# Performance work log

Measured on AMD Instinct MI355X. Metric: run time of the kernel, lower is better.

## Reference

```python
import jax, jax.numpy as jnp
import numpy as np

N_GRIDS, N_FEATS = 64, 2
GD = GH = GW = 64
PE_TERMS, N_DIMS = 6, 3
NODES, N_OUT = 64, 1
N_PTS = 524288


def setup_inputs() -> dict:
    key = jax.random.key(0)
    ks = jax.random.split(key, 8)
    x = jax.random.uniform(ks[0], (N_PTS, N_DIMS), jnp.float32, -1.0, 1.0)
    grid_scales = jax.random.uniform(ks[1], (N_GRIDS, 3), jnp.float32, 1.0, 4.0)
    grid_translations = jax.random.uniform(ks[2], (N_GRIDS, 3), jnp.float32, -1.0, 1.0) * (grid_scales - 1.0)
    feature_grids = jax.random.normal(ks[3], (N_GRIDS, N_FEATS, GD, GH, GW), jnp.float32)
    d_in = PE_TERMS * N_DIMS * 2 + N_FEATS * N_GRIDS  # 36 + 128 = 164
    W0 = jax.random.normal(ks[4], (d_in, NODES), jnp.float32) * np.sqrt(2.0 / (d_in + NODES))
    b0 = jnp.zeros((NODES,), jnp.float32)
    W1 = jax.random.normal(ks[5], (NODES, NODES), jnp.float32) * np.sqrt(2.0 / (2 * NODES))
    b1 = jnp.zeros((NODES,), jnp.float32)
    W2 = jax.random.normal(ks[6], (NODES, N_OUT), jnp.float32) * np.sqrt(2.0 / (NODES + N_OUT))
    b2 = jnp.zeros((N_OUT,), jnp.float32)
    return dict(x=x, grid_scales=grid_scales, grid_translations=grid_translations,
                feature_grids=feature_grids, W0=W0, b0=b0, W1=W1, b1=b1, W2=W2, b2=b2)


def grid_sample_3d(vol, coords):
    """Trilinear grid_sample, align_corners=True, padding_mode='zeros'.
    vol: [C,D,H,W]; coords: [N,3] in (x,y,z) order (x -> W axis), range [-1,1].
    Returns [C,N]."""
    C, D, H, W = vol.shape
    flat = vol.reshape(C, D * H * W)
    ix = (coords[:, 0] + 1.0) * 0.5 * (W - 1)
    iy = (coords[:, 1] + 1.0) * 0.5 * (H - 1)
    iz = (coords[:, 2] + 1.0) * 0.5 * (D - 1)
    x0 = jnp.floor(ix); y0 = jnp.floor(iy); z0 = jnp.floor(iz)
    wx = ix - x0; wy = iy - y0; wz = iz - z0
    x0i = x0.astype(jnp.int32); y0i = y0.astype(jnp.int32); z0i = z0.astype(jnp.int32)
    out = jnp.zeros((C, coords.shape[0]), vol.dtype)
    for dz, wz_ in ((0, 1.0 - wz), (1, wz)):
        for dy, wy_ in ((0, 1.0 - wy), (1, wy)):
            for dx, wx_ in ((0, 1.0 - wx), (1, wx)):
                xi = x0i + dx; yi = y0i + dy; zi = z0i + dz
                valid = (xi >= 0) & (xi < W) & (yi >= 0) & (yi < H) & (zi >= 0) & (zi < D)
                idx = (jnp.clip(zi, 0, D - 1) * H + jnp.clip(yi, 0, H - 1)) * W + jnp.clip(xi, 0, W - 1)
                v = jnp.take(flat, idx, axis=1) * valid.astype(vol.dtype)[None, :]
                out = out + v * (wz_ * wy_ * wx_)[None, :]
    return out


def positional_encoding(x):
    # NeRF-style PE: sin/cos of pi*2^i * x, i in [0, PE_TERMS), out dim = 2*L*3
    freqs = jnp.pi * (2.0 ** jnp.arange(PE_TERMS, dtype=jnp.float32))  # [L]
    ang = x[:, None, :] * freqs[None, :, None]                          # [N,L,3]
    n = x.shape[0]
    return jnp.concatenate([jnp.sin(ang).reshape(n, -1), jnp.cos(ang).reshape(n, -1)], axis=1)


def snake_alt(x):
    return 0.5 * x + jnp.sin(x) ** 2


def reference(x, grid_scales, grid_translations, feature_grids, W0, b0, W1, b1, W2, b2):
    # per-grid affine transform (equivalent to bmm with the scale+translation 4x4)
    tp = x[None, :, :] * grid_scales[:, None, :] + grid_translations[:, None, :]  # [G,N,3]
    feats = jax.vmap(grid_sample_3d)(feature_grids, tp)  # [G,C,N]
    G, C, N = feats.shape
    feats = feats.reshape(G * C, N).T                    # [N, G*C]
    pe = positional_encoding(x)                          # [N, 2*L*3]
    y = jnp.concatenate([pe, feats], axis=1)
    y = snake_alt(y @ W0 + b0)
    y = snake_alt(y @ W1 + b1)
    y = y @ W2 + b2
    return y
```

## Files before the change

kernel.cpp:

```cpp
#include <hip/hip_runtime.h>
#include <hip/hip_bf16.h>

#define NPTS    524288
#define NG      64
#define GSZ     64
#define VOX     (GSZ*GSZ*GSZ)
#define NODES   64
#define TILE    64
#define NBLK    (NPTS / TILE)
#define K0      192
#define SF      200
#define WLCAP   2048
#define NCELL   4096

typedef __attribute__((ext_vector_type(8))) short bf16x8;
typedef __attribute__((ext_vector_type(4))) float f32x4;

__device__ inline unsigned short f2bf(float f) {
    __hip_bfloat16 b = __float2bfloat16(f);
    union { __hip_bfloat16 h; unsigned short u; } cv; cv.h = b;
    return cv.u;
}
__device__ inline unsigned int pk2(float c0, float c1) {
    return (unsigned int)f2bf(c0) | ((unsigned int)f2bf(c1) << 16);
}
__device__ inline float bflo(unsigned int v) { return __uint_as_float(v << 16); }
__device__ inline float bfhi(unsigned int v) { return __uint_as_float(v & 0xffff0000u); }

__device__ inline int spread4(int v) {
    return (v & 1) | ((v & 2) << 2) | ((v & 4) << 4) | ((v & 8) << 6);
}
__device__ inline int cell_of(float px, float py, float pz) {
    int cx = min(max((int)((px + 1.0f) * 8.0f), 0), 15);
    int cy = min(max((int)((py + 1.0f) * 8.0f), 0), 15);
    int cz = min(max((int)((pz + 1.0f) * 8.0f), 0), 15);
    return spread4(cx) | (spread4(cy) << 1) | (spread4(cz) << 2);
}

__global__ void vox_prep(const float* __restrict__ fg, uint4* __restrict__ vox4) {
    int idx = blockIdx.x * blockDim.x + threadIdx.x;
    int g = idx >> 16;
    int v = (idx & 65535) * 4;
    const float* base = fg + (size_t)g * (2 * VOX) + v;
    float4 a = *(const float4*)base;
    float4 b = *(const float4*)(base + VOX);
    vox4[idx] = make_uint4(pk2(a.x, b.x), pk2(a.y, b.y), pk2(a.z, b.z), pk2(a.w, b.w));
}

__global__ void w_prep(const float* __restrict__ W0, const float* __restrict__ W1,
                       unsigned short* __restrict__ w0t, unsigned short* __restrict__ w1t,
                       int* __restrict__ hist) {
    int t = blockIdx.x * blockDim.x + threadIdx.x;
    hist[t] = 0;
    for (int i = t; i < NODES * K0; i += 4096) {
        int n = i / K0, k = i - n * K0;
        w0t[i] = (k < 164) ? f2bf(W0[k * NODES + n]) : (unsigned short)0;
    }
    for (int i = t; i < NODES * NODES; i += 4096) {
        int n = i >> 6, k = i & 63;
        w1t[i] = f2bf(W1[k * NODES + n]);
    }
}

__global__ void sort_count(const float* __restrict__ x, unsigned short* __restrict__ cell_id,
                           int* __restrict__ hist) {
    int p = blockIdx.x * blockDim.x + threadIdx.x;
    int c = cell_of(x[p * 3 + 0], x[p * 3 + 1], x[p * 3 + 2]);
    cell_id[p] = (unsigned short)c;
    atomicAdd(&hist[c], 1);
}

__global__ void sort_scan(const int* __restrict__ hist, int* __restrict__ offs) {
    __shared__ int partial[256];
    int t = threadIdx.x;
    int loc[16];
    int s = 0;
    #pragma unroll
    for (int i = 0; i < 16; ++i) { loc[i] = s; s += hist[t * 16 + i]; }
    partial[t] = s;
    __syncthreads();
    for (int d = 1; d < 256; d <<= 1) {
        int v = (t >= d) ? partial[t - d] : 0;
        __syncthreads();
        partial[t] += v;
        __syncthreads();
    }
    int base = partial[t] - s;
    #pragma unroll
    for (int i = 0; i < 16; ++i) offs[t * 16 + i] = base + loc[i];
}

__global__ void sort_scatter(const float* __restrict__ x, const unsigned short* __restrict__ cell_id,
                             int* __restrict__ offs, float4* __restrict__ spts) {
    int p = blockIdx.x * blockDim.x + threadIdx.x;
    int c = cell_id[p];
    int pos = atomicAdd(&offs[c], 1);
    spts[pos] = make_float4(x[p * 3 + 0], x[p * 3 + 1], x[p * 3 + 2], __int_as_float(p));
}

__device__ inline void gather_pair(int pt, int g,
                                   const unsigned int* __restrict__ vox,
                                   const float* xs, const float* gss, const float* gts,
                                   unsigned short* Fsh) {
    float px = xs[pt * 3 + 0], py = xs[pt * 3 + 1], pz = xs[pt * 3 + 2];
    float ix = (px * gss[g * 3 + 0] + gts[g * 3 + 0] + 1.0f) * 31.5f;
    float iy = (py * gss[g * 3 + 1] + gts[g * 3 + 1] + 1.0f) * 31.5f;
    float iz = (pz * gss[g * 3 + 2] + gts[g * 3 + 2] + 1.0f) * 31.5f;
    float fx = floorf(ix), fy = floorf(iy), fz = floorf(iz);
    int x0 = (int)fx, y0 = (int)fy, z0 = (int)fz;
    float wx = ix - fx, wy = iy - fy, wz = iz - fz;
    float wxa0 = (x0 >= 0) ? (1.0f - wx) : 0.0f;
    float wxa1 = (x0 < 63) ? wx : 0.0f;
    float wya0 = (y0 >= 0) ? (1.0f - wy) : 0.0f;
    float wya1 = (y0 < 63) ? wy : 0.0f;
    float wza0 = (z0 >= 0) ? (1.0f - wz) : 0.0f;
    float wza1 = (z0 < 63) ? wz : 0.0f;
    int xc0 = max(x0, 0), xc1 = min(x0 + 1, 63);
    int yc0 = max(y0, 0), yc1 = min(y0 + 1, 63);
    int zc0 = max(z0, 0), zc1 = min(z0 + 1, 63);
    const unsigned int* vg = vox + ((size_t)g << 18);
    float f0 = 0.f, f1 = 0.f;
    #pragma unroll
    for (int dz = 0; dz < 2; ++dz) {
        int zc = dz ? zc1 : zc0; float wzv = dz ? wza1 : wza0;
        #pragma unroll
        for (int dy = 0; dy < 2; ++dy) {
            int yc = dy ? yc1 : yc0; float wyv = dy ? wya1 : wya0;
            int rowb = ((zc << 6) + yc) << 6;
            float wzy = wzv * wyv;
            unsigned int v0 = vg[rowb + xc0], v1 = vg[rowb + xc1];
            f0 += wzy * (wxa0 * bflo(v0) + wxa1 * bflo(v1));
            f1 += wzy * (wxa0 * bfhi(v0) + wxa1 * bfhi(v1));
        }
    }
    *(unsigned int*)&Fsh[pt * SF + 36 + 2 * g] = pk2(f0, f1);
}

__global__ void __launch_bounds__(256, 5)
amrsrn_main(const float4* __restrict__ spts,
            const float* __restrict__ gscale,
            const float* __restrict__ gtrans,
            const unsigned int* __restrict__ vox,
            const unsigned short* __restrict__ w0t,
            const unsigned short* __restrict__ w1t,
            const float* __restrict__ b0,
            const float* __restrict__ b1,
            const float* __restrict__ W2,
            const float* __restrict__ b2,
            float* __restrict__ out) {
    __shared__ unsigned short Fsh[TILE * SF];
    __shared__ unsigned short wl[WLCAP];
    __shared__ float xs[TILE * 3];
    __shared__ int   sidx[TILE];
    __shared__ float gss[NG * 3];
    __shared__ float gts[NG * 3];
    __shared__ int wl_cnt;

    const int tid = threadIdx.x;
    const int lane = tid & 63;
    const int cb = ((blockIdx.x & 7) << 10) | (blockIdx.x >> 3);
    const int base = cb * TILE;

    for (int i = tid; i < TILE * SF / 8; i += 256) ((uint4*)Fsh)[i] = make_uint4(0,0,0,0);
    if (tid < TILE) {
        float4 sp = spts[base + tid];
        xs[tid * 3 + 0] = sp.x; xs[tid * 3 + 1] = sp.y; xs[tid * 3 + 2] = sp.z;
        sidx[tid] = __float_as_int(sp.w);
    }
    if (tid < NG * 3) { gss[tid] = gscale[tid]; gts[tid] = gtrans[tid]; }
    if (tid == 0) wl_cnt = 0;
    __syncthreads();

    {
        int pt = tid & 63;
        int grp = tid >> 6;
        #pragma unroll
        for (int t = 0; t < 9; ++t) {
            int tau = grp * 9 + t;
            int tt = (tau < 18) ? tau : tau - 18;
            int l = tt / 3, d = tt - l * 3;
            float ang = xs[pt * 3 + d] * (3.14159265358979323846f * (float)(1 << l));
            float val = (tau < 18) ? __sinf(ang) : __cosf(ang);
            Fsh[pt * SF + tau] = f2bf(val);
        }
    }

    {
        int pt = tid & 63;
        int gbase = (tid >> 6) * 16;
        float px = xs[pt * 3 + 0], py = xs[pt * 3 + 1], pz = xs[pt * 3 + 2];
        for (int gi = 0; gi < 16; ++gi) {
            int g = gbase + gi;
            float ix = (px * gss[g * 3 + 0] + gts[g * 3 + 0] + 1.0f) * 31.5f;
            float iy = (py * gss[g * 3 + 1] + gts[g * 3 + 1] + 1.0f) * 31.5f;
            float iz = (pz * gss[g * 3 + 2] + gts[g * 3 + 2] + 1.0f) * 31.5f;
            bool valid = (ix >= -1.0f) & (ix < 64.0f)
                       & (iy >= -1.0f) & (iy < 64.0f)
                       & (iz >= -1.0f) & (iz < 64.0f);
            unsigned long long m = __ballot(valid);
            if (m) {
                int b = 0;
                if (lane == 0) b = atomicAdd(&wl_cnt, __popcll(m));
                b = __shfl(b, 0);
                if (valid) {
                    int slot = b + __popcll(m & ((1ull << lane) - 1ull));
                    if (slot < WLCAP) wl[slot] = (unsigned short)((pt << 6) | g);
                    else gather_pair(pt, g, vox, xs, gss, gts, Fsh);
                }
            }
        }
    }
    __syncthreads();

    {
        int n = min(wl_cnt, WLCAP);
        for (int i = tid; i < n; i += 256) {
            int e = wl[i];
            gather_pair(e >> 6, e & 63, vox, xs, gss, gts, Fsh);
        }
    }
    __syncthreads();

    const int wv = tid >> 6;
    const int ptb = wv * 16;
    const int row = lane & 15;
    const int quad = lane >> 4;
    const int koff = quad * 8;

    f32x4 acc0[4] = {{0,0,0,0},{0,0,0,0},{0,0,0,0},{0,0,0,0}};
    #pragma unroll
    for (int ks = 0; ks < 6; ++ks) {
        bf16x8 a = *(const bf16x8*)&Fsh[(ptb + row) * SF + ks * 32 + koff];
        #pragma unroll
        for (int nt = 0; nt < 4; ++nt) {
            bf16x8 b = *(const bf16x8*)&w0t[(nt * 16 + row) * K0 + ks * 32 + koff];
            acc0[nt] = __builtin_amdgcn_mfma_f32_16x16x32_bf16(a, b, acc0[nt], 0, 0, 0);
        }
    }
    #pragma unroll
    for (int nt = 0; nt < 4; ++nt) {
        int node = nt * 16 + row;
        float bb = b0[node];
        #pragma unroll
        for (int r = 0; r < 4; ++r) {
            float h = acc0[nt][r] + bb;
            float s = __sinf(h);
            h = 0.5f * h + s * s;
            Fsh[(ptb + quad * 4 + r) * SF + node] = f2bf(h);
        }
    }

    f32x4 acc1[4] = {{0,0,0,0},{0,0,0,0},{0,0,0,0},{0,0,0,0}};
    #pragma unroll
    for (int ks = 0; ks < 2; ++ks) {
        bf16x8 a = *(const bf16x8*)&Fsh[(ptb + row) * SF + ks * 32 + koff];
        #pragma unroll
        for (int nt = 0; nt < 4; ++nt) {
            bf16x8 b = *(const bf16x8*)&w1t[(nt * 16 + row) * NODES + ks * 32 + koff];
            acc1[nt] = __builtin_amdgcn_mfma_f32_16x16x32_bf16(a, b, acc1[nt], 0, 0, 0);
        }
    }
    float part[4] = {0.f, 0.f, 0.f, 0.f};
    #pragma unroll
    for (int nt = 0; nt < 4; ++nt) {
        int node = nt * 16 + row;
        float b1v = b1[node];
        float w2v = W2[node];
        #pragma unroll
        for (int r = 0; r < 4; ++r) {
            float h = acc1[nt][r] + b1v;
            float s = __sinf(h);
            h = 0.5f * h + s * s;
            part[r] += h * w2v;
        }
    }
    #pragma unroll
    for (int m = 1; m < 16; m <<= 1) {
        #pragma unroll
        for (int r = 0; r < 4; ++r) part[r] += __shfl_xor(part[r], m);
    }
    if (row == 0) {
        float b2v = b2[0];
        #pragma unroll
        for (int r = 0; r < 4; ++r) {
            int pt = ptb + quad * 4 + r;
            out[sidx[pt]] = part[r] + b2v;
        }
    }
}

__global__ void amrsrn_fallback(const float* __restrict__ x,
                                const float* __restrict__ gscale,
                                const float* __restrict__ gtrans,
                                const float* __restrict__ fg,
                                const float* __restrict__ W0,
                                const float* __restrict__ b0,
                                const float* __restrict__ W1,
                                const float* __restrict__ b1,
                                const float* __restrict__ W2,
                                const float* __restrict__ b2,
                                float* __restrict__ out) {
    int p = blockIdx.x * blockDim.x + threadIdx.x;
    float px = x[p*3+0], py = x[p*3+1], pz = x[p*3+2];
    float h0[NODES];
    #pragma unroll
    for (int j = 0; j < NODES; ++j) h0[j] = b0[j];
    #pragma unroll
    for (int l = 0; l < 6; ++l) {
        float freq = 3.14159265358979323846f * (float)(1 << l);
        #pragma unroll
        for (int d = 0; d < 3; ++d) {
            float v = (d == 0 ? px : (d == 1 ? py : pz)) * freq;
            float s = __sinf(v), c = __cosf(v);
            const float* wrs = W0 + (l*3 + d) * NODES;
            const float* wrc = W0 + (18 + l*3 + d) * NODES;
            #pragma unroll
            for (int j = 0; j < NODES; ++j) h0[j] += s * wrs[j] + c * wrc[j];
        }
    }
    for (int g = 0; g < NG; ++g) {
        float ix = (px * gscale[g*3+0] + gtrans[g*3+0] + 1.0f) * 31.5f;
        float iy = (py * gscale[g*3+1] + gtrans[g*3+1] + 1.0f) * 31.5f;
        float iz = (pz * gscale[g*3+2] + gtrans[g*3+2] + 1.0f) * 31.5f;
        float fxf = floorf(ix), fyf = floorf(iy), fzf = floorf(iz);
        int x0 = (int)fxf, y0 = (int)fyf, z0 = (int)fzf;
        float wx = ix - fxf, wy = iy - fyf, wz = iz - fzf;
        bool any = (x0 >= -1 && x0 < GSZ) && (y0 >= -1 && y0 < GSZ) && (z0 >= -1 && z0 < GSZ);
        if (any) {
            float f0 = 0.f, f1 = 0.f;
            #pragma unroll
            for (int dz = 0; dz < 2; ++dz) {
                int zi = z0 + dz; bool vz = ((unsigned)zi < (unsigned)GSZ);
                int zc = min(max(zi, 0), GSZ - 1);
                float wzf = dz ? wz : 1.f - wz;
                #pragma unroll
                for (int dy = 0; dy < 2; ++dy) {
                    int yi = y0 + dy; bool vy = ((unsigned)yi < (unsigned)GSZ);
                    int yc = min(max(yi, 0), GSZ - 1);
                    float wyf = dy ? wy : 1.f - wy;
                    int rowoff = (zc * GSZ + yc) * GSZ;
                    #pragma unroll
                    for (int dx = 0; dx < 2; ++dx) {
                        int xi = x0 + dx; bool vx = ((unsigned)xi < (unsigned)GSZ);
                        int xc = min(max(xi, 0), GSZ - 1);
                        float w = wzf * wyf * (dx ? wx : 1.f - wx);
                        w = (vz && vy && vx) ? w : 0.f;
                        const float* gp = fg + ((size_t)g << 19);
                        f0 += w * gp[rowoff + xc];
                        f1 += w * gp[VOX + rowoff + xc];
                    }
                }
            }
            const float* wr = W0 + (36 + 2*g) * NODES;
            #pragma unroll
            for (int j = 0; j < NODES; ++j) h0[j] += f0 * wr[j] + f1 * wr[NODES + j];
        }
    }
    #pragma unroll
    for (int j = 0; j < NODES; ++j) { float s = __sinf(h0[j]); h0[j] = 0.5f * h0[j] + s * s; }
    float out_acc = b2[0];
    #pragma unroll
    for (int half = 0; half < 2; ++half) {
        float h1[32];
        #pragma unroll
        for (int j = 0; j < 32; ++j) h1[j] = b1[half*32 + j];
        #pragma unroll
        for (int i = 0; i < NODES; ++i) {
            float a = h0[i];
            const float* w1r = W1 + i * NODES + half*32;
            #pragma unroll
            for (int j = 0; j < 32; ++j) h1[j] += a * w1r[j];
        }
        #pragma unroll
        for (int j = 0; j < 32; ++j) { float s = __sinf(h1[j]); out_acc += (0.5f * h1[j] + s * s) * W2[half*32 + j]; }
    }
    out[p] = out_acc;
}

extern "C" void kernel_launch(void* const* d_in, const int* in_sizes, int n_in,
                              void* d_out, int out_size, void* d_ws, size_t ws_size,
                              hipStream_t stream) {
    const float* x      = (const float*)d_in[0];
    const float* gscale = (const float*)d_in[1];
    const float* gtrans = (const float*)d_in[2];
    const float* fg     = (const float*)d_in[3];
    const float* W0     = (const float*)d_in[4];
    const float* b0     = (const float*)d_in[5];
    const float* W1     = (const float*)d_in[6];
    const float* b1     = (const float*)d_in[7];
    const float* W2     = (const float*)d_in[8];
    const float* b2     = (const float*)d_in[9];
    float* out = (float*)d_out;

    char* wsp = (char*)d_ws;
    unsigned short* w0t = (unsigned short*)wsp;
    unsigned short* w1t = w0t + NODES * K0;
    int* hist           = (int*)(wsp + (64 << 10));
    int* offs           = (int*)(wsp + (80 << 10));
    unsigned short* cid = (unsigned short*)(wsp + (96 << 10));
    float4* spts        = (float4*)(wsp + (96 << 10) + (1 << 20));
    unsigned int* vox   = (unsigned int*)(wsp + (96 << 10) + (1 << 20) + (8 << 20));
    const size_t ws_needed = (96 << 10) + (1 << 20) + (8 << 20) + (size_t)NG * VOX * 4;

    if (ws_size >= ws_needed) {
        vox_prep<<<(NG * VOX / 4) / 256, 256, 0, stream>>>(fg, (uint4*)vox);
        w_prep<<<16, 256, 0, stream>>>(W0, W1, w0t, w1t, hist);
        sort_count<<<NPTS / 256, 256, 0, stream>>>(x, cid, hist);
        sort_scan<<<1, 256, 0, stream>>>(hist, offs);
        sort_scatter<<<NPTS / 256, 256, 0, stream>>>(x, cid, offs, spts);
        amrsrn_main<<<NBLK, 256, 0, stream>>>(spts, gscale, gtrans, vox,
                                              w0t, w1t, b0, b1, W2, b2, out);
    } else {
        amrsrn_fallback<<<NPTS / 256, 256, 0, stream>>>(
            x, gscale, gtrans, fg, W0, b0, W1, b1, W2, b2, out);
    }
}
```

Baseline: 473.5 us.

## Replace per-point gather worklist with per-cell grid masks and batched gathers

Precomputes, for each of 4096 spatial cells, a 64-bit mask of which grids can overlap that cell. The main kernel ORs the masks over the tile's cell range and gathers only from those grids, dropping the per-point ballot/atomic worklist. Gathers are split into address prep, eight loads and math, and two pairs are issued together to raise memory-level parallelism. Launches are fused (weight prep with mask build, voxel packing with scatter) and the cell id is packed into the point index so the cid array is no longer needed. The tile-level union mask may include many grids that are invalid for individual points, so some useless gathers can be added.

```diff
diff --git a/kernel.cpp b/kernel.cpp
--- a/kernel.cpp
+++ b/kernel.cpp
@@ -10,7 +10,6 @@
 #define NBLK    (NPTS / TILE)
 #define K0      192
 #define SF      200
-#define WLCAP   2048
 #define NCELL   4096
 
 typedef __attribute__((ext_vector_type(8))) short bf16x8;
@@ -29,6 +28,9 @@
 
 __device__ inline int spread4(int v) {
     return (v & 1) | ((v & 2) << 2) | ((v & 4) << 4) | ((v & 8) << 6);
+}
+__device__ inline int compact4(int v) {
+    return (v & 1) | ((v >> 2) & 2) | ((v >> 4) & 4) | ((v >> 6) & 8);
 }
 __device__ inline int cell_of(float px, float py, float pz) {
     int cx = min(max((int)((px + 1.0f) * 8.0f), 0), 15);
@@ -37,36 +39,45 @@
     return spread4(cx) | (spread4(cy) << 1) | (spread4(cz) << 2);
 }
 
-__global__ void vox_prep(const float* __restrict__ fg, uint4* __restrict__ vox4) {
-    int idx = blockIdx.x * blockDim.x + threadIdx.x;
-    int g = idx >> 16;
-    int v = (idx & 65535) * 4;
-    const float* base = fg + (size_t)g * (2 * VOX) + v;
-    float4 a = *(const float4*)base;
-    float4 b = *(const float4*)(base + VOX);
-    vox4[idx] = make_uint4(pk2(a.x, b.x), pk2(a.y, b.y), pk2(a.z, b.z), pk2(a.w, b.w));
-}
-
-__global__ void w_prep(const float* __restrict__ W0, const float* __restrict__ W1,
-                       unsigned short* __restrict__ w0t, unsigned short* __restrict__ w1t,
-                       int* __restrict__ hist) {
-    int t = blockIdx.x * blockDim.x + threadIdx.x;
-    hist[t] = 0;
-    for (int i = t; i < NODES * K0; i += 4096) {
-        int n = i / K0, k = i - n * K0;
-        w0t[i] = (k < 164) ? f2bf(W0[k * NODES + n]) : (unsigned short)0;
-    }
-    for (int i = t; i < NODES * NODES; i += 4096) {
-        int n = i >> 6, k = i & 63;
-        w1t[i] = f2bf(W1[k * NODES + n]);
-    }
-}
-
-__global__ void sort_count(const float* __restrict__ x, unsigned short* __restrict__ cell_id,
-                           int* __restrict__ hist) {
+__global__ void prep_small(const float* __restrict__ W0, const float* __restrict__ W1,
+                           const float* __restrict__ gscale, const float* __restrict__ gtrans,
+                           unsigned short* __restrict__ w0t, unsigned short* __restrict__ w1t,
+                           int* __restrict__ hist, uint2* __restrict__ masks) {
+    int bid = blockIdx.x, tid = threadIdx.x;
+    if (bid < 16) {
+        int t = bid * 256 + tid;
+        hist[t] = 0;
+        for (int i = t; i < NODES * K0; i += 4096) {
+            int n = i / K0, k = i - n * K0;
+            w0t[i] = (k < 164) ? f2bf(W0[k * NODES + n]) : (unsigned short)0;
+        }
+        for (int i = t; i < NODES * NODES; i += 4096) {
+            int n = i >> 6, k = i & 63;
+            w1t[i] = f2bf(W1[k * NODES + n]);
+        }
+    } else {
+        int cell = (bid - 16) * 4 + (tid >> 6);
+        if (cell >= NCELL) return;
+        int g = tid & 63;
+        int cx = compact4(cell), cy = compact4(cell >> 1), cz = compact4(cell >> 2);
+        float lo[3] = { -1.0f + cx * 0.125f, -1.0f + cy * 0.125f, -1.0f + cz * 0.125f };
+        const float LOB = -1.0318f - 1e-4f, HIB = 1.0318f + 1e-4f;
+        bool ok = true;
+        #pragma unroll
+        for (int a = 0; a < 3; ++a) {
+            float s = gscale[g * 3 + a], t = gtrans[g * 3 + a];
+            float cA = s * lo[a] + t, cB = s * (lo[a] + 0.125f) + t;
+            float cmin = fminf(cA, cB), cmax = fmaxf(cA, cB);
+            ok = ok && (cmax >= LOB) && (cmin <= HIB);
+        }
+        unsigned long long m = __ballot(ok);
+        if (g == 0) masks[cell] = make_uint2((unsigned int)m, (unsigned int)(m >> 32));
+    }
+}
+
+__global__ void sort_count(const float* __restrict__ x, int* __restrict__ hist) {
     int p = blockIdx.x * blockDim.x + threadIdx.x;
     int c = cell_of(x[p * 3 + 0], x[p * 3 + 1], x[p * 3 + 2]);
-    cell_id[p] = (unsigned short)c;
     atomicAdd(&hist[c], 1);
 }
 
@@ -90,50 +101,81 @@
     for (int i = 0; i < 16; ++i) offs[t * 16 + i] = base + loc[i];
 }
 
-__global__ void sort_scatter(const float* __restrict__ x, const unsigned short* __restrict__ cell_id,
-                             int* __restrict__ offs, float4* __restrict__ spts) {
-    int p = blockIdx.x * blockDim.x + threadIdx.x;
-    int c = cell_id[p];
-    int pos = atomicAdd(&offs[c], 1);
-    spts[pos] = make_float4(x[p * 3 + 0], x[p * 3 + 1], x[p * 3 + 2], __int_as_float(p));
-}
-
-__device__ inline void gather_pair(int pt, int g,
-                                   const unsigned int* __restrict__ vox,
-                                   const float* xs, const float* gss, const float* gts,
-                                   unsigned short* Fsh) {
-    float px = xs[pt * 3 + 0], py = xs[pt * 3 + 1], pz = xs[pt * 3 + 2];
-    float ix = (px * gss[g * 3 + 0] + gts[g * 3 + 0] + 1.0f) * 31.5f;
-    float iy = (py * gss[g * 3 + 1] + gts[g * 3 + 1] + 1.0f) * 31.5f;
-    float iz = (pz * gss[g * 3 + 2] + gts[g * 3 + 2] + 1.0f) * 31.5f;
+__global__ void prep_big(const float* __restrict__ fg, uint4* __restrict__ vox4,
+                         const float* __restrict__ x, int* __restrict__ offs,
+                         float4* __restrict__ spts) {
+    int bid = blockIdx.x, tid = threadIdx.x;
+    if (bid < 16384) {
+        int idx = bid * 256 + tid;
+        int g = idx >> 16;
+        int v = (idx & 65535) * 4;
+        const float* base = fg + (size_t)g * (2 * VOX) + v;
+        float4 a = *(const float4*)base;
+        float4 b = *(const float4*)(base + VOX);
+        vox4[idx] = make_uint4(pk2(a.x, b.x), pk2(a.y, b.y), pk2(a.z, b.z), pk2(a.w, b.w));
+    } else {
+        int p = (bid - 16384) * 256 + tid;
+        float px = x[p * 3 + 0], py = x[p * 3 + 1], pz = x[p * 3 + 2];
+        int c = cell_of(px, py, pz);
+        int pos = atomicAdd(&offs[c], 1);
+        spts[pos] = make_float4(px, py, pz, __int_as_float(p | (c << 19)));
+    }
+}
+
+struct Pre {
+    const unsigned int* r0; const unsigned int* r1;
+    const unsigned int* r2; const unsigned int* r3;
+    int x0o, x1o, dst;
+    float wzy0, wzy1, wzy2, wzy3, wx0, wx1;
+};
+
+__device__ inline void prep_pair(int pt, int g, const float* xs,
+                                 const float* gss, const float* gts,
+                                 const unsigned int* __restrict__ vox, Pre& P) {
+    float ix = (xs[pt * 3 + 0] * gss[g * 3 + 0] + gts[g * 3 + 0] + 1.0f) * 31.5f;
+    float iy = (xs[pt * 3 + 1] * gss[g * 3 + 1] + gts[g * 3 + 1] + 1.0f) * 31.5f;
+    float iz = (xs[pt * 3 + 2] * gss[g * 3 + 2] + gts[g * 3 + 2] + 1.0f) * 31.5f;
     float fx = floorf(ix), fy = floorf(iy), fz = floorf(iz);
     int x0 = (int)fx, y0 = (int)fy, z0 = (int)fz;
     float wx = ix - fx, wy = iy - fy, wz = iz - fz;
-    float wxa0 = (x0 >= 0) ? (1.0f - wx) : 0.0f;
-    float wxa1 = (x0 < 63) ? wx : 0.0f;
-    float wya0 = (y0 >= 0) ? (1.0f - wy) : 0.0f;
-    float wya1 = (y0 < 63) ? wy : 0.0f;
-    float wza0 = (z0 >= 0) ? (1.0f - wz) : 0.0f;
-    float wza1 = (z0 < 63) ? wz : 0.0f;
-    int xc0 = max(x0, 0), xc1 = min(x0 + 1, 63);
-    int yc0 = max(y0, 0), yc1 = min(y0 + 1, 63);
-    int zc0 = max(z0, 0), zc1 = min(z0 + 1, 63);
+    float wxa0 = ((unsigned)x0 < 64u) ? (1.0f - wx) : 0.0f;
+    float wxa1 = ((unsigned)(x0 + 1) < 64u) ? wx : 0.0f;
+    float wya0 = ((unsigned)y0 < 64u) ? (1.0f - wy) : 0.0f;
+    float wya1 = ((unsigned)(y0 + 1) < 64u) ? wy : 0.0f;
+    float wza0 = ((unsigned)z0 < 64u) ? (1.0f - wz) : 0.0f;
+    float wza1 = ((unsigned)(z0 + 1) < 64u) ? wz : 0.0f;
+    int xc0 = min(max(x0, 0), 63), xc1 = min(max(x0 + 1, 0), 63);
+    int yc0 = min(max(y0, 0), 63), yc1 = min(max(y0 + 1, 0), 63);
+    int zc0 = min(max(z0, 0), 63), zc1 = min(max(z0 + 1, 0), 63);
     const unsigned int* vg = vox + ((size_t)g << 18);
-    float f0 = 0.f, f1 = 0.f;
-    #pragma unroll
-    for (int dz = 0; dz < 2; ++dz) {
-        int zc = dz ? zc1 : zc0; float wzv = dz ? wza1 : wza0;
-        #pragma unroll
-        for (int dy = 0; dy < 2; ++dy) {
-            int yc = dy ? yc1 : yc0; float wyv = dy ? wya1 : wya0;
-            int rowb = ((zc << 6) + yc) << 6;
-            float wzy = wzv * wyv;
-            unsigned int v0 = vg[rowb + xc0], v1 = vg[rowb + xc1];
-            f0 += wzy * (wxa0 * bflo(v0) + wxa1 * bflo(v1));
-            f1 += wzy * (wxa0 * bfhi(v0) + wxa1 * bfhi(v1));
-        }
-    }
-    *(unsigned int*)&Fsh[pt * SF + 36 + 2 * g] = pk2(f0, f1);
+    P.r0 = vg + (((zc0 << 6) + yc0) << 6);
+    P.r1 = vg + (((zc0 << 6) + yc1) << 6);
+    P.r2 = vg + (((zc1 << 6) + yc0) << 6);
+    P.r3 = vg + (((zc1 << 6) + yc1) << 6);
+    P.wzy0 = wza0 * wya0; P.wzy1 = wza0 * wya1;
+    P.wzy2 = wza1 * wya0; P.wzy3 = wza1 * wya1;
+    P.x0o = xc0; P.x1o = xc1;
+    P.wx0 = wxa0; P.wx1 = wxa1;
+    P.dst = pt * SF + 36 + 2 * g;
+}
+
+__device__ inline void load8(const Pre& P, unsigned int* v) {
+    v[0] = P.r0[P.x0o]; v[1] = P.r0[P.x1o];
+    v[2] = P.r1[P.x0o]; v[3] = P.r1[P.x1o];
+    v[4] = P.r2[P.x0o]; v[5] = P.r2[P.x1o];
+    v[6] = P.r3[P.x0o]; v[7] = P.r3[P.x1o];
+}
+
+__device__ inline void math_pair(const Pre& P, const unsigned int* v, unsigned short* Fsh) {
+    float f0 = P.wzy0 * (P.wx0 * bflo(v[0]) + P.wx1 * bflo(v[1]))
+             + P.wzy1 * (P.wx0 * bflo(v[2]) + P.wx1 * bflo(v[3]))
+             + P.wzy2 * (P.wx0 * bflo(v[4]) + P.wx1 * bflo(v[5]))
+             + P.wzy3 * (P.wx0 * bflo(v[6]) + P.wx1 * bflo(v[7]));
+    float f1 = P.wzy0 * (P.wx0 * bfhi(v[0]) + P.wx1 * bfhi(v[1]))
+             + P.wzy1 * (P.wx0 * bfhi(v[2]) + P.wx1 * bfhi(v[3]))
+             + P.wzy2 * (P.wx0 * bfhi(v[4]) + P.wx1 * bfhi(v[5]))
+             + P.wzy3 * (P.wx0 * bfhi(v[6]) + P.wx1 * bfhi(v[7]));
+    *(unsigned int*)&Fsh[P.dst] = pk2(f0, f1);
 }
 
 __global__ void __launch_bounds__(256, 5)
@@ -141,6 +183,7 @@
             const float* __restrict__ gscale,
             const float* __restrict__ gtrans,
             const unsigned int* __restrict__ vox,
+            const uint2* __restrict__ masks,
             const unsigned short* __restrict__ w0t,
             const unsigned short* __restrict__ w1t,
             const float* __restrict__ b0,
@@ -149,26 +192,26 @@
             const float* __restrict__ b2,
             float* __restrict__ out) {
     __shared__ unsigned short Fsh[TILE * SF];
-    __shared__ unsigned short wl[WLCAP];
     __shared__ float xs[TILE * 3];
-    __shared__ int   sidx[TILE];
+    __shared__ int   sraw[TILE];
     __shared__ float gss[NG * 3];
     __shared__ float gts[NG * 3];
-    __shared__ int wl_cnt;
+    __shared__ unsigned int bm[2];
+    __shared__ unsigned char glist[NG];
 
     const int tid = threadIdx.x;
     const int lane = tid & 63;
     const int cb = ((blockIdx.x & 7) << 10) | (blockIdx.x >> 3);
     const int base = cb * TILE;
 
-    for (int i = tid; i < TILE * SF / 8; i += 256) ((uint4*)Fsh)[i] = make_uint4(0,0,0,0);
+    for (int i = tid; i < TILE * SF / 8; i += 256) ((uint4*)Fsh)[i] = make_uint4(0, 0, 0, 0);
     if (tid < TILE) {
         float4 sp = spts[base + tid];
         xs[tid * 3 + 0] = sp.x; xs[tid * 3 + 1] = sp.y; xs[tid * 3 + 2] = sp.z;
-        sidx[tid] = __float_as_int(sp.w);
+        sraw[tid] = __float_as_int(sp.w);
     }
     if (tid < NG * 3) { gss[tid] = gscale[tid]; gts[tid] = gtrans[tid]; }
-    if (tid == 0) wl_cnt = 0;
+    if (tid < 2) bm[tid] = 0;
     __syncthreads();
 
     {
@@ -183,40 +226,34 @@
             float val = (tau < 18) ? __sinf(ang) : __cosf(ang);
             Fsh[pt * SF + tau] = f2bf(val);
         }
-    }
+        unsigned int c0 = ((unsigned int)sraw[0]) >> 19;
+        unsigned int c1 = ((unsigned int)sraw[TILE - 1]) >> 19;
+        for (unsigned int c = c0 + tid; c <= c1; c += 256) {
+            uint2 m = masks[c];
+            atomicOr(&bm[0], m.x);
+            atomicOr(&bm[1], m.y);
+        }
+    }
+    __syncthreads();
+
+    unsigned long long mask = (unsigned long long)bm[0] | ((unsigned long long)bm[1] << 32);
+    int ng = __popcll(mask);
+    if (tid < NG && ((mask >> tid) & 1ull))
+        glist[__popcll(mask & ((1ull << tid) - 1ull))] = (unsigned char)tid;
+    __syncthreads();
 
     {
-        int pt = tid & 63;
-        int gbase = (tid >> 6) * 16;
-        float px = xs[pt * 3 + 0], py = xs[pt * 3 + 1], pz = xs[pt * 3 + 2];
-        for (int gi = 0; gi < 16; ++gi) {
-            int g = gbase + gi;
-            float ix = (px * gss[g * 3 + 0] + gts[g * 3 + 0] + 1.0f) * 31.5f;
-            float iy = (py * gss[g * 3 + 1] + gts[g * 3 + 1] + 1.0f) * 31.5f;
-            float iz = (pz * gss[g * 3 + 2] + gts[g * 3 + 2] + 1.0f) * 31.5f;
-            bool valid = (ix >= -1.0f) & (ix < 64.0f)
-                       & (iy >= -1.0f) & (iy < 64.0f)
-                       & (iz >= -1.0f) & (iz < 64.0f);
-            unsigned long long m = __ballot(valid);
-            if (m) {
-                int b = 0;
-                if (lane == 0) b = atomicAdd(&wl_cnt, __popcll(m));
-                b = __shfl(b, 0);
-                if (valid) {
-                    int slot = b + __popcll(m & ((1ull << lane) - 1ull));
-                    if (slot < WLCAP) wl[slot] = (unsigned short)((pt << 6) | g);
-                    else gather_pair(pt, g, vox, xs, gss, gts, Fsh);
-                }
-            }
-        }
-    }
-    __syncthreads();
-
-    {
-        int n = min(wl_cnt, WLCAP);
-        for (int i = tid; i < n; i += 256) {
-            int e = wl[i];
-            gather_pair(e >> 6, e & 63, vox, xs, gss, gts, Fsh);
+        int n64 = ng << 6;
+        for (int i = tid; i < n64; i += 512) {
+            int j = (i + 256 < n64) ? i + 256 : i;
+            Pre A, B;
+            prep_pair(i & 63, glist[i >> 6], xs, gss, gts, vox, A);
+            prep_pair(j & 63, glist[j >> 6], xs, gss, gts, vox, B);
+            unsigned int va[8], vb[8];
+            load8(A, va);
+            load8(B, vb);
+            math_pair(A, va, Fsh);
+            math_pair(B, vb, Fsh);
         }
     }
     __syncthreads();
@@ -284,7 +321,7 @@
         #pragma unroll
         for (int r = 0; r < 4; ++r) {
             int pt = ptb + quad * 4 + r;
-            out[sidx[pt]] = part[r] + b2v;
+            out[sraw[pt] & 0x7FFFF] = part[r] + b2v;
         }
     }
 }
@@ -394,21 +431,20 @@
 
     char* wsp = (char*)d_ws;
     unsigned short* w0t = (unsigned short*)wsp;
-    unsigned short* w1t = w0t + NODES * K0;
-    int* hist           = (int*)(wsp + (64 << 10));
-    int* offs           = (int*)(wsp + (80 << 10));
-    unsigned short* cid = (unsigned short*)(wsp + (96 << 10));
-    float4* spts        = (float4*)(wsp + (96 << 10) + (1 << 20));
-    unsigned int* vox   = (unsigned int*)(wsp + (96 << 10) + (1 << 20) + (8 << 20));
-    const size_t ws_needed = (96 << 10) + (1 << 20) + (8 << 20) + (size_t)NG * VOX * 4;
+    unsigned short* w1t = (unsigned short*)(wsp + 24576);
+    int* hist           = (int*)(wsp + 32768);
+    int* offs           = (int*)(wsp + 49152);
+    uint2* masks        = (uint2*)(wsp + 65536);
+    float4* spts        = (float4*)(wsp + (1 << 20));
+    unsigned int* vox   = (unsigned int*)(wsp + (9 << 20));
+    const size_t ws_needed = (size_t)(9 << 20) + (size_t)NG * VOX * 4;
 
     if (ws_size >= ws_needed) {
-        vox_prep<<<(NG * VOX / 4) / 256, 256, 0, stream>>>(fg, (uint4*)vox);
-        w_prep<<<16, 256, 0, stream>>>(W0, W1, w0t, w1t, hist);
-        sort_count<<<NPTS / 256, 256, 0, stream>>>(x, cid, hist);
+        prep_small<<<16 + NCELL / 4, 256, 0, stream>>>(W0, W1, gscale, gtrans, w0t, w1t, hist, masks);
+        sort_count<<<NPTS / 256, 256, 0, stream>>>(x, hist);
         sort_scan<<<1, 256, 0, stream>>>(hist, offs);
-        sort_scatter<<<NPTS / 256, 256, 0, stream>>>(x, cid, offs, spts);
-        amrsrn_main<<<NBLK, 256, 0, stream>>>(spts, gscale, gtrans, vox,
+        prep_big<<<16384 + NPTS / 256, 256, 0, stream>>>(fg, (uint4*)vox, x, offs, spts);
+        amrsrn_main<<<NBLK, 256, 0, stream>>>(spts, gscale, gtrans, vox, masks,
                                               w0t, w1t, b0, b1, W2, b2, out);
     } else {
         amrsrn_fallback<<<NPTS / 256, 256, 0, stream>>>(
```

Measured after the change: 498.1 us. +5.2%, slower.
